# Kernel tuning notes

Measured on AMD Instinct MI355X. Metric: run time of the kernel, lower is better.

Reference implementation:

```python
import jax, jax.numpy as jnp
import numpy as np

N = 8192
IN_DIM = 256
HID = 256
OUT_DIM = 256
P_DIM = 3
SIGMA = 1.0


def setup_inputs() -> dict:
    key = jax.random.key(0)
    ks = jax.random.split(key, 7)
    s_in = 1.0 / np.sqrt(IN_DIM)
    inp = {
        "X": jax.random.normal(ks[0], (N, IN_DIM + P_DIM), dtype=jnp.float32),
        "WQ": jax.random.uniform(ks[1], (IN_DIM, HID), jnp.float32, -s_in, s_in),
        "bQ": jax.random.uniform(ks[2], (HID,), jnp.float32, -s_in, s_in),
        "WK": jax.random.uniform(ks[3], (IN_DIM, HID), jnp.float32, -s_in, s_in),
        "bK": jax.random.uniform(ks[4], (HID,), jnp.float32, -s_in, s_in),
        "WV": jax.random.uniform(ks[5], (IN_DIM, OUT_DIM), jnp.float32, -s_in, s_in),
        "bV": jax.random.uniform(ks[6], (OUT_DIM,), jnp.float32, -s_in, s_in),
    }
    return inp


def _softmax_one(x):
    # exp(x - max) / (1 + sum(exp(x - max))) -- faithful to the torch softmax_one
    m = jnp.max(x, axis=-1, keepdims=True)
    e = jnp.exp(x - m)
    return e / (1.0 + jnp.sum(e, axis=-1, keepdims=True))


def reference(X, WQ, bQ, WK, bK, WV, bV):
    P = X[:, -P_DIM:]            # [N, 3] spatial coords
    Xf = X[:, :-P_DIM]           # [N, IN_DIM] features

    Q = Xf @ WQ + bQ             # [N, HID]
    K = Xf @ WK + bK             # [N, HID]
    V = Xf @ WV + bV             # [N, OUT_DIM]

    scores = (Q @ K.T) / jnp.sqrt(jnp.asarray(HID, Xf.dtype))  # [N, N]

    # squared pairwise distances ||P_i - P_j||^2 (cdist(P,P)**2)
    sq = jnp.sum(P * P, axis=-1)                                # [N]
    d2 = jnp.maximum(sq[:, None] + sq[None, :] - 2.0 * (P @ P.T), 0.0)
    decay = jnp.exp(-d2 / (2.0 * SIGMA ** 2))                   # [N, N]

    A = _softmax_one(scores * decay)                             # [N, N]
    H = A @ V                                                    # [N, OUT_DIM]
    # residual: input_dim == output_dim so res_proj is None
    return H + Xf
```

## Files before the change

kernel.cpp:

```cpp
#include <hip/hip_runtime.h>
#include <hip/hip_bf16.h>
#include <stdint.h>

#define NTOK 8192
#define XSTRIDE 259
#define LOG2E 1.4426950408889634f
#define DECC (-3.4712336270551023f)
#define BN 32

typedef __bf16 bf16x8 __attribute__((ext_vector_type(8)));
typedef float f32x4 __attribute__((ext_vector_type(4)));
typedef float f32x16 __attribute__((ext_vector_type(16)));
typedef unsigned short u16;

union BF8 { u16 u[8]; bf16x8 v; };
union PW  { uint32_t u[4]; bf16x8 v; };

__device__ __forceinline__ u16 f2bf(float f) {
  uint32_t u = __float_as_uint(f);
  u += 0x7FFFu + ((u >> 16) & 1u);
  return (u16)(u >> 16);
}
__device__ __forceinline__ float bf2f(u16 h) {
  return __uint_as_float(((uint32_t)h) << 16);
}
__device__ __forceinline__ float exp2_hw(float x) {
  float r; asm("v_exp_f32 %0, %1" : "=v"(r) : "v"(x)); return r;
}
__device__ __forceinline__ f32x4 mfma16(bf16x8 a, bf16x8 b, f32x4 c) {
  return __builtin_amdgcn_mfma_f32_16x16x32_bf16(a, b, c, 0, 0, 0);
}
__device__ __forceinline__ f32x16 mfma32(bf16x8 a, bf16x8 b, f32x16 c) {
  return __builtin_amdgcn_mfma_f32_32x32x16_bf16(a, b, c, 0, 0, 0);
}
__device__ __forceinline__ void async16(const void* g, void* l) {
  __builtin_amdgcn_global_load_lds(
      (const __attribute__((address_space(1))) uint32_t*)g,
      (__attribute__((address_space(3))) uint32_t*)l, 16, 0, 0);
}
__device__ __forceinline__ void bsplit(float v, u16& h, u16& l) {
  h = f2bf(v);
  l = f2bf(v - bf2f(h));
}

__global__ __launch_bounds__(256) void pos_kernel(
    const float* __restrict__ X, u16* __restrict__ Qp, u16* __restrict__ Kp) {
  const int r = blockIdx.x * 256 + threadIdx.x;
  const float* xp = X + (size_t)r * XSTRIDE + 256;
  const float x = xp[0], y = xp[1], z = xp[2];
  const float w = 0.5f * (x * x + y * y + z * z);
  u16 xh, xl, yh, yl, zh, zl, wh, wl;
  bsplit(x, xh, xl); bsplit(y, yh, yl); bsplit(z, zh, zl); bsplit(w, wh, wl);
  const u16 one = 0x3F80u;
  const u16 SGN = 0x8000u;
  union { u16 u[16]; uint4 v4[2]; } uq, uk;
  uq.u[0] = wh;  uk.u[0] = one;
  uq.u[1] = wl;  uk.u[1] = one;
  uq.u[2] = one; uk.u[2] = wh;
  uq.u[3] = one; uk.u[3] = wl;
  uq.u[4] = (u16)(xh ^ SGN); uk.u[4] = xh;
  uq.u[5] = (u16)(xh ^ SGN); uk.u[5] = xl;
  uq.u[6] = (u16)(xl ^ SGN); uk.u[6] = xh;
  uq.u[7] = (u16)(yh ^ SGN); uk.u[7] = yh;
  uq.u[8] = (u16)(yh ^ SGN); uk.u[8] = yl;
  uq.u[9] = (u16)(yl ^ SGN); uk.u[9] = yh;
  uq.u[10] = (u16)(zh ^ SGN); uk.u[10] = zh;
  uq.u[11] = (u16)(zh ^ SGN); uk.u[11] = zl;
  uq.u[12] = (u16)(zl ^ SGN); uk.u[12] = zh;
  uq.u[13] = 0; uk.u[13] = 0;
  uq.u[14] = 0; uk.u[14] = 0;
  uq.u[15] = 0; uk.u[15] = 0;
  ((uint4*)Qp)[r * 2] = uq.v4[0];
  ((uint4*)Qp)[r * 2 + 1] = uq.v4[1];
  ((uint4*)Kp)[r * 2] = uk.v4[0];
  ((uint4*)Kp)[r * 2 + 1] = uk.v4[1];
}

__global__ __launch_bounds__(256) void xb_kernel(
    const float* __restrict__ X, u16* __restrict__ Xb) {
  const int t = threadIdx.x;
  const int row = blockIdx.x * 8 + (t >> 5);
  const int c0 = (t & 31) * 8;
  const float* xp = X + (size_t)row * XSTRIDE + c0;
  union { u16 u[8]; uint4 v; } o;
#pragma unroll
  for (int j = 0; j < 8; ++j) o.u[j] = f2bf(xp[j]);
  *(uint4*)(Xb + (size_t)row * 256 + c0) = o.v;
}

__global__ __launch_bounds__(256) void wprep_kernel(
    const float* __restrict__ WQ, const float* __restrict__ WK,
    const float* __restrict__ WV, u16* __restrict__ Wt) {
  const int o = blockIdx.x;
  const int which = o >> 8, oo = o & 255;
  const float* W = (which == 0) ? WQ : ((which == 1) ? WK : WV);
  const int k = threadIdx.x;
  Wt[(size_t)o * 256 + k] = f2bf(W[(size_t)k * 256 + oo]);
}

__global__ __launch_bounds__(256) void qkv_kernel(
    const u16* __restrict__ Xb, const u16* __restrict__ Wt,
    const float* __restrict__ bQ, const float* __restrict__ bK,
    const float* __restrict__ bV,
    u16* __restrict__ Qb, u16* __restrict__ Kb, u16* __restrict__ Vt) {
  __shared__ u16 wt[64 * 256];
  const int tid = threadIdx.x;
  const int lane = tid & 63;
  const int wave = tid >> 6;
  const int l15 = lane & 15;
  const int q4 = lane >> 4;
  const int rb = blockIdx.x;
  const int ch = blockIdx.y;
  const int which = ch >> 2;
  const int c0 = (ch & 3) * 64;
  const float* bias = (which == 0) ? bQ : ((which == 1) ? bK : bV);

  bf16x8 xa[2][8];
#pragma unroll
  for (int mt = 0; mt < 2; ++mt) {
    const int row = rb * 128 + wave * 32 + mt * 16 + l15;
#pragma unroll
    for (int kc = 0; kc < 8; ++kc)
      xa[mt][kc] = *(const bf16x8*)(Xb + (size_t)row * 256 + kc * 32 + q4 * 8);
  }
  {
    const u16* Wsrc = Wt + (size_t)(which * 256 + c0) * 256;
    const int rb0 = wave * 16;
#pragma unroll
    for (int i = 0; i < 8; ++i) {
      int r = rb0 + i * 2 + (lane >> 5);
      int c = (lane & 31) ^ (r & 7);
      async16(Wsrc + (size_t)r * 256 + c * 8, wt + (rb0 + i * 2) * 256);
    }
  }
  asm volatile("s_waitcnt vmcnt(0)" ::: "memory");
  __syncthreads();

  f32x4 acc[2][4];
#pragma unroll
  for (int mt = 0; mt < 2; ++mt)
#pragma unroll
    for (int nt = 0; nt < 4; ++nt) acc[mt][nt] = (f32x4){0.f, 0.f, 0.f, 0.f};

#pragma unroll
  for (int kc = 0; kc < 8; ++kc) {
#pragma unroll
    for (int nt = 0; nt < 4; ++nt) {
      bf16x8 wf = *(const bf16x8*)(wt + (nt * 16 + l15) * 256 +
                                   (((kc * 4 + q4) ^ (l15 & 7)) * 8));
#pragma unroll
      for (int mt = 0; mt < 2; ++mt)
        acc[mt][nt] = mfma16(xa[mt][kc], wf, acc[mt][nt]);
    }
  }
  float bc[4];
#pragma unroll
  for (int nt = 0; nt < 4; ++nt) bc[nt] = bias[c0 + nt * 16 + l15];

#pragma unroll
  for (int mt = 0; mt < 2; ++mt)
#pragma unroll
    for (int nt = 0; nt < 4; ++nt)
#pragma unroll
      for (int r = 0; r < 4; ++r) {
        float v = acc[mt][nt][r] + bc[nt];
        int grow = rb * 128 + wave * 32 + mt * 16 + q4 * 4 + r;
        int gc = c0 + nt * 16 + l15;
        if (which == 2)      Vt[(size_t)gc * NTOK + grow] = f2bf(v);
        else if (which == 1) Kb[(size_t)grow * 256 + gc] = f2bf(v);
        else                 Qb[(size_t)((grow >> 5) * 16 + (gc >> 4)) * 512 +
                                ((gc >> 3) & 1) * 256 + (grow & 31) * 8 +
                                (gc & 7)] = f2bf(v);
      }
}

template<int KS>
__global__ __launch_bounds__((KS == 16) ? 512 : 256, 2) void attn_kernel(
    const u16* __restrict__ Qb, const u16* __restrict__ Kb,
    const u16* __restrict__ Vt, const u16* __restrict__ Qp,
    const u16* __restrict__ Kp, u16* __restrict__ Op,
    float* __restrict__ ml) {
  constexpr int WPB = (KS == 16) ? 8 : 4;
  constexpr int KW  = WPB / 2;
  constexpr int SPL = NTOK / KS;
  constexpr int NIT = SPL / BN;
  constexpr int IK  = BN / KW / 2;
  constexpr int FPW = 256 / KW;
  constexpr int IV  = FPW / 16;

  __shared__ u16 kbuf[2][BN * 256];
  __shared__ u16 vbuf[2][256 * BN];
  __shared__ u16 kpbuf[2][BN * 16];

  const int tid = threadIdx.x;
  const int lane = tid & 63;
  const int wave = tid >> 6;
  const int l31 = lane & 31;
  const int h5 = lane >> 5;
  const int sp = blockIdx.x;
  const int rb = blockIdx.y;
  const int q0 = rb * (32 * WPB);
  const int wrow = wave * 32;

#define STAGE(T)                                                              \
  do {                                                                        \
    const int key0_ = sp * SPL + (T) * BN;                                    \
    const int b_ = (T) & 1;                                                   \
    if (wave < KW) {                                                          \
      const int rb0 = wave * (BN / KW);                                       \
      _Pragma("unroll")                                                       \
      for (int i = 0; i < IK; ++i) {                                          \
        int r = rb0 + i * 2 + (lane >> 5);                                    \
        int c = (lane & 31) ^ (r & 7);                                        \
        async16(Kb + (size_t)(key0_ + r) * 256 + c * 8,                       \
                &kbuf[b_][(rb0 + i * 2) * 256]);                              \
      }                                                                       \
      if (wave == 1)                                                          \
        async16(Kp + (size_t)(key0_ + (lane >> 1)) * 16 + (lane & 1) * 8,     \
                &kpbuf[b_][0]);                                               \
    } else {                                                                  \
      const int fb0 = (wave - KW) * FPW;                                      \
      _Pragma("unroll")                                                       \
      for (int i = 0; i < IV; ++i) {                                          \
        int f = fb0 + i * 16 + (lane >> 2);                                   \
        int c = (lane & 3) ^ ((f >> 1) & 3);                                  \
        async16(Vt + (size_t)f * NTOK + key0_ + c * 8,                        \
                &vbuf[b_][(fb0 + i * 16) * 32]);                              \
      }                                                                       \
    }                                                                         \
  } while (0)

  const int rb32 = rb * WPB + wave;
  bf16x8 qa[16];
#pragma unroll
  for (int kc = 0; kc < 16; ++kc)
    qa[kc] = *(const bf16x8*)(Qb + ((size_t)(rb32 * 16 + kc) * 64 + lane) * 8);

  const bf16x8 qp = *(const bf16x8*)(Qp + (size_t)(q0 + wrow + l31) * 16 +
                                     h5 * 8);

  f32x16 O[8];
#pragma unroll
  for (int ft = 0; ft < 8; ++ft)
#pragma unroll
    for (int r = 0; r < 16; ++r) O[ft][r] = 0.f;
  float lrow = 0.f;

  const int kswz = l31 & 7;
  const int vswz = (l31 >> 1) & 3;

  STAGE(0);

#pragma unroll 1
  for (int it = 0; it < NIT; ++it) {
    const int cur = it & 1;
    asm volatile("s_waitcnt vmcnt(0)" ::: "memory");
    __syncthreads();

    const int nx = (it + 1 < NIT) ? (it + 1) : (NIT - 1);
    STAGE(nx);

    f32x16 T;
#pragma unroll
    for (int r = 0; r < 16; ++r) T[r] = 0.f;
    {
      bf16x8 kpf = *(const bf16x8*)(&kpbuf[cur][l31 * 16 + h5 * 8]);
      T = mfma32(kpf, qp, T);
    }

    f32x16 S;
#pragma unroll
    for (int r = 0; r < 16; ++r) S[r] = 0.f;
    __builtin_amdgcn_s_setprio(1);
#pragma unroll
    for (int kc = 0; kc < 16; ++kc) {
      bf16x8 kf = *(const bf16x8*)(&kbuf[cur][l31 * 256 +
                                   (((2 * kc + h5) ^ kswz) * 8)]);
      S = mfma32(kf, qa[kc], S);
    }
    __builtin_amdgcn_s_setprio(0);

#pragma unroll
    for (int r = 0; r < 16; ++r) {
      float dec = exp2_hw(fmaf(T[r], -LOG2E, DECC));
      float p = exp2_hw(S[r] * dec);
      S[r] = p;
      lrow += p;
    }

    uint32_t w0, w1, w2, w3, w4, w5, w6, w7;
    asm("v_cvt_pk_bf16_f32 %0, %1, %2" : "=v"(w0) : "v"(S[0]),  "v"(S[1]));
    asm("v_cvt_pk_bf16_f32 %0, %1, %2" : "=v"(w1) : "v"(S[2]),  "v"(S[3]));
    asm("v_cvt_pk_bf16_f32 %0, %1, %2" : "=v"(w2) : "v"(S[4]),  "v"(S[5]));
    asm("v_cvt_pk_bf16_f32 %0, %1, %2" : "=v"(w3) : "v"(S[6]),  "v"(S[7]));
    asm("v_cvt_pk_bf16_f32 %0, %1, %2" : "=v"(w4) : "v"(S[8]),  "v"(S[9]));
    asm("v_cvt_pk_bf16_f32 %0, %1, %2" : "=v"(w5) : "v"(S[10]), "v"(S[11]));
    asm("v_cvt_pk_bf16_f32 %0, %1, %2" : "=v"(w6) : "v"(S[12]), "v"(S[13]));
    asm("v_cvt_pk_bf16_f32 %0, %1, %2" : "=v"(w7) : "v"(S[14]), "v"(S[15]));
    asm volatile("v_permlane32_swap_b32 %0, %1" : "+v"(w2), "+v"(w0));
    asm volatile("v_permlane32_swap_b32 %0, %1" : "+v"(w3), "+v"(w1));
    asm volatile("v_permlane32_swap_b32 %0, %1" : "+v"(w6), "+v"(w4));
    asm volatile("v_permlane32_swap_b32 %0, %1" : "+v"(w7), "+v"(w5));
    PW pa0, pa1;
    pa0.u[0] = w0; pa0.u[1] = w1; pa0.u[2] = w2; pa0.u[3] = w3;
    pa1.u[0] = w4; pa1.u[1] = w5; pa1.u[2] = w6; pa1.u[3] = w7;

    __builtin_amdgcn_s_setprio(1);
#pragma unroll
    for (int kh = 0; kh < 2; ++kh) {
      const bf16x8 pa = kh ? pa1.v : pa0.v;
#pragma unroll
      for (int ft = 0; ft < 8; ++ft) {
        bf16x8 vf = *(const bf16x8*)(&vbuf[cur][(ft * 32 + l31) * 32 +
                                     (((2 * kh + h5) ^ vswz) * 8)]);
        O[ft] = mfma32(pa, vf, O[ft]);
      }
    }
    __builtin_amdgcn_s_setprio(0);
  }

  float lsum = lrow + __shfl_xor(lrow, 32);
#pragma unroll
  for (int ft = 0; ft < 8; ++ft)
#pragma unroll
    for (int r = 0; r < 16; ++r) {
      int row = q0 + wrow + (r & 3) + 8 * (r >> 2) + 4 * h5;
      Op[((size_t)sp * NTOK + row) * 256 + ft * 32 + l31] = f2bf(O[ft][r]);
    }
  if (lane < 32)
    ml[sp * NTOK + q0 + wrow + lane] = lsum;
#undef STAGE
}

template<int KS>
__global__ __launch_bounds__(256) void combine_kernel(
    const float* __restrict__ X, const u16* __restrict__ Op,
    const float* __restrict__ ml, float* __restrict__ out) {
  const int row = blockIdx.x;
  const int f = threadIdx.x;
  float den = 1.f, num = 0.f;
#pragma unroll
  for (int s = 0; s < KS; ++s) {
    den += ml[s * NTOK + row];
    num += bf2f(Op[((size_t)s * NTOK + row) * 256 + f]);
  }
  out[(size_t)row * 256 + f] = num / den + X[(size_t)row * XSTRIDE + f];
}

extern "C" void kernel_launch(void* const* d_in, const int* in_sizes, int n_in,
                              void* d_out, int out_size, void* d_ws, size_t ws_size,
                              hipStream_t stream) {
  (void)in_sizes; (void)n_in; (void)out_size;
  const float* X  = (const float*)d_in[0];
  const float* WQ = (const float*)d_in[1];
  const float* bQ = (const float*)d_in[2];
  const float* WK = (const float*)d_in[3];
  const float* bK = (const float*)d_in[4];
  const float* WV = (const float*)d_in[5];
  const float* bV = (const float*)d_in[6];
  float* out = (float*)d_out;
  char* ws = (char*)d_ws;

  u16*   Qb = (u16*)(ws);
  u16*   Kb = (u16*)(ws + ((size_t)4 << 20));
  u16*   Vt = (u16*)(ws + ((size_t)8 << 20));
  u16*   Qp = (u16*)(ws + ((size_t)12 << 20));
  u16*   Kp = (u16*)(ws + ((size_t)12 << 20) + 262144);
  u16*   Wt = (u16*)(ws + ((size_t)12 << 20) + 524288);
  u16*   Xb = (u16*)(ws + ((size_t)12 << 20) + 524288 + 393216);
  float* ml = (float*)(ws + ((size_t)16 << 20) + 524288 + 393216);
  u16*   Op = (u16*)(ws + ((size_t)16 << 20) + 524288 + 393216 + 524288);

  const size_t op_off = ((size_t)16 << 20) + 524288 + 393216 + 524288;
  const size_t need16 = op_off + (size_t)16 * NTOK * 256 * 2;
  const bool big = (ws_size >= need16);

  pos_kernel<<<dim3(NTOK / 256), dim3(256), 0, stream>>>(X, Qp, Kp);
  xb_kernel<<<dim3(NTOK / 8), dim3(256), 0, stream>>>(X, Xb);
  wprep_kernel<<<dim3(768), dim3(256), 0, stream>>>(WQ, WK, WV, Wt);
  qkv_kernel<<<dim3(64, 12), dim3(256), 0, stream>>>(Xb, Wt, bQ, bK, bV,
                                                     Qb, Kb, Vt);
  if (big) {
    attn_kernel<16><<<dim3(16, NTOK / 256), dim3(512), 0, stream>>>(
        Qb, Kb, Vt, Qp, Kp, Op, ml);
    combine_kernel<16><<<dim3(NTOK), dim3(256), 0, stream>>>(X, Op, ml, out);
  } else {
    attn_kernel<8><<<dim3(8, NTOK / 128), dim3(256), 0, stream>>>(
        Qb, Kb, Vt, Qp, Kp, Op, ml);
    combine_kernel<8><<<dim3(NTOK), dim3(256), 0, stream>>>(X, Op, ml, out);
  }
}
```

Before: 224.7 us.

## Triple-buffer attention K/V staging with all waves loading and fixed 8-way split

The attention kernel now keeps three LDS buffers and prefetches two tiles ahead. It uses partial vmcnt waits and a plain s_barrier in place of a full drain plus __syncthreads. All eight waves now share K and V loads, where before half the waves loaded K and half loaded V. The key split is fixed at 8 with 256-row blocks, which halves the grid compared with the earlier 16-split path and removes the workspace-size branch. This aims to hide global load latency better, at the cost of more LDS per block (which may limit occupancy) and less grid parallelism.

```diff
diff --git a/kernel.cpp b/kernel.cpp
--- a/kernel.cpp
+++ b/kernel.cpp
@@ -6,7 +6,10 @@
 #define XSTRIDE 259
 #define LOG2E 1.4426950408889634f
 #define DECC (-3.4712336270551023f)
+#define KSPLIT 8
+#define SPLEN (NTOK / KSPLIT)
 #define BN 32
+#define ITERS (SPLEN / BN)
 
 typedef __bf16 bf16x8 __attribute__((ext_vector_type(8)));
 typedef float f32x4 __attribute__((ext_vector_type(4)));
@@ -174,23 +177,14 @@
       }
 }
 
-template<int KS>
-__global__ __launch_bounds__((KS == 16) ? 512 : 256, 2) void attn_kernel(
+__global__ __launch_bounds__(512, 2) void attn_kernel(
     const u16* __restrict__ Qb, const u16* __restrict__ Kb,
     const u16* __restrict__ Vt, const u16* __restrict__ Qp,
     const u16* __restrict__ Kp, u16* __restrict__ Op,
     float* __restrict__ ml) {
-  constexpr int WPB = (KS == 16) ? 8 : 4;
-  constexpr int KW  = WPB / 2;
-  constexpr int SPL = NTOK / KS;
-  constexpr int NIT = SPL / BN;
-  constexpr int IK  = BN / KW / 2;
-  constexpr int FPW = 256 / KW;
-  constexpr int IV  = FPW / 16;
-
-  __shared__ u16 kbuf[2][BN * 256];
-  __shared__ u16 vbuf[2][256 * BN];
-  __shared__ u16 kpbuf[2][BN * 16];
+  __shared__ u16 kbuf[3][BN * 256];
+  __shared__ u16 vbuf[3][256 * BN];
+  __shared__ u16 kpbuf[3][BN * 16];
 
   const int tid = threadIdx.x;
   const int lane = tid & 63;
@@ -199,38 +193,32 @@
   const int h5 = lane >> 5;
   const int sp = blockIdx.x;
   const int rb = blockIdx.y;
-  const int q0 = rb * (32 * WPB);
+  const int q0 = rb * 256;
   const int wrow = wave * 32;
 
-#define STAGE(T)                                                              \
+#define STAGE(T, S_)                                                          \
   do {                                                                        \
-    const int key0_ = sp * SPL + (T) * BN;                                    \
-    const int b_ = (T) & 1;                                                   \
-    if (wave < KW) {                                                          \
-      const int rb0 = wave * (BN / KW);                                       \
-      _Pragma("unroll")                                                       \
-      for (int i = 0; i < IK; ++i) {                                          \
-        int r = rb0 + i * 2 + (lane >> 5);                                    \
-        int c = (lane & 31) ^ (r & 7);                                        \
-        async16(Kb + (size_t)(key0_ + r) * 256 + c * 8,                       \
-                &kbuf[b_][(rb0 + i * 2) * 256]);                              \
-      }                                                                       \
-      if (wave == 1)                                                          \
-        async16(Kp + (size_t)(key0_ + (lane >> 1)) * 16 + (lane & 1) * 8,     \
-                &kpbuf[b_][0]);                                               \
-    } else {                                                                  \
-      const int fb0 = (wave - KW) * FPW;                                      \
-      _Pragma("unroll")                                                       \
-      for (int i = 0; i < IV; ++i) {                                          \
-        int f = fb0 + i * 16 + (lane >> 2);                                   \
-        int c = (lane & 3) ^ ((f >> 1) & 3);                                  \
-        async16(Vt + (size_t)f * NTOK + key0_ + c * 8,                        \
-                &vbuf[b_][(fb0 + i * 16) * 32]);                              \
-      }                                                                       \
+    const int key0_ = sp * SPLEN + (T) * BN;                                  \
+    _Pragma("unroll")                                                         \
+    for (int j = 0; j < 2; ++j) {                                             \
+      int r = wave * 4 + j * 2 + (lane >> 5);                                 \
+      int c = (lane & 31) ^ (r & 7);                                          \
+      async16(Kb + (size_t)(key0_ + r) * 256 + c * 8,                         \
+              &kbuf[S_][(wave * 4 + j * 2) * 256]);                           \
     }                                                                         \
+    _Pragma("unroll")                                                         \
+    for (int j = 0; j < 2; ++j) {                                             \
+      int f = wave * 32 + j * 16 + (lane >> 2);                               \
+      int c = (lane & 3) ^ ((f >> 1) & 3);                                    \
+      async16(Vt + (size_t)f * NTOK + key0_ + c * 8,                          \
+              &vbuf[S_][(wave * 32 + j * 16) * 32]);                          \
+    }                                                                         \
+    if (wave == 0)                                                            \
+      async16(Kp + (size_t)(key0_ + (lane >> 1)) * 16 + (lane & 1) * 8,       \
+              &kpbuf[S_][0]);                                                 \
   } while (0)
 
-  const int rb32 = rb * WPB + wave;
+  const int rb32 = rb * 8 + wave;
   bf16x8 qa[16];
 #pragma unroll
   for (int kc = 0; kc < 16; ++kc)
@@ -249,16 +237,24 @@
   const int kswz = l31 & 7;
   const int vswz = (l31 >> 1) & 3;
 
-  STAGE(0);
-
+  STAGE(0, 0);
+  STAGE(1, 1);
+
+  int cur = 0;
 #pragma unroll 1
-  for (int it = 0; it < NIT; ++it) {
-    const int cur = it & 1;
-    asm volatile("s_waitcnt vmcnt(0)" ::: "memory");
-    __syncthreads();
-
-    const int nx = (it + 1 < NIT) ? (it + 1) : (NIT - 1);
-    STAGE(nx);
+  for (int t = 0; t < ITERS; ++t) {
+    if (t + 1 < ITERS) {
+      if (wave == 0) asm volatile("s_waitcnt vmcnt(5)" ::: "memory");
+      else           asm volatile("s_waitcnt vmcnt(4)" ::: "memory");
+    } else {
+      asm volatile("s_waitcnt vmcnt(0)" ::: "memory");
+    }
+    __builtin_amdgcn_s_barrier();
+
+    if (t + 2 < ITERS) {
+      const int s2 = (cur >= 1) ? (cur - 1) : 2;
+      STAGE(t + 2, s2);
+    }
 
     f32x16 T;
 #pragma unroll
@@ -317,6 +313,8 @@
       }
     }
     __builtin_amdgcn_s_setprio(0);
+
+    cur = (cur == 2) ? 0 : (cur + 1);
   }
 
   float lsum = lrow + __shfl_xor(lrow, 32);
@@ -332,7 +330,6 @@
 #undef STAGE
 }
 
-template<int KS>
 __global__ __launch_bounds__(256) void combine_kernel(
     const float* __restrict__ X, const u16* __restrict__ Op,
     const float* __restrict__ ml, float* __restrict__ out) {
@@ -340,7 +337,7 @@
   const int f = threadIdx.x;
   float den = 1.f, num = 0.f;
 #pragma unroll
-  for (int s = 0; s < KS; ++s) {
+  for (int s = 0; s < KSPLIT; ++s) {
     den += ml[s * NTOK + row];
     num += bf2f(Op[((size_t)s * NTOK + row) * 256 + f]);
   }
@@ -350,7 +347,7 @@
 extern "C" void kernel_launch(void* const* d_in, const int* in_sizes, int n_in,
                               void* d_out, int out_size, void* d_ws, size_t ws_size,
                               hipStream_t stream) {
-  (void)in_sizes; (void)n_in; (void)out_size;
+  (void)in_sizes; (void)n_in; (void)out_size; (void)ws_size;
   const float* X  = (const float*)d_in[0];
   const float* WQ = (const float*)d_in[1];
   const float* bQ = (const float*)d_in[2];
@@ -371,22 +368,12 @@
   float* ml = (float*)(ws + ((size_t)16 << 20) + 524288 + 393216);
   u16*   Op = (u16*)(ws + ((size_t)16 << 20) + 524288 + 393216 + 524288);
 
-  const size_t op_off = ((size_t)16 << 20) + 524288 + 393216 + 524288;
-  const size_t need16 = op_off + (size_t)16 * NTOK * 256 * 2;
-  const bool big = (ws_size >= need16);
-
   pos_kernel<<<dim3(NTOK / 256), dim3(256), 0, stream>>>(X, Qp, Kp);
   xb_kernel<<<dim3(NTOK / 8), dim3(256), 0, stream>>>(X, Xb);
   wprep_kernel<<<dim3(768), dim3(256), 0, stream>>>(WQ, WK, WV, Wt);
   qkv_kernel<<<dim3(64, 12), dim3(256), 0, stream>>>(Xb, Wt, bQ, bK, bV,
                                                      Qb, Kb, Vt);
-  if (big) {
-    attn_kernel<16><<<dim3(16, NTOK / 256), dim3(512), 0, stream>>>(
-        Qb, Kb, Vt, Qp, Kp, Op, ml);
-    combine_kernel<16><<<dim3(NTOK), dim3(256), 0, stream>>>(X, Op, ml, out);
-  } else {
-    attn_kernel<8><<<dim3(8, NTOK / 128), dim3(256), 0, stream>>>(
-        Qb, Kb, Vt, Qp, Kp, Op, ml);
-    combine_kernel<8><<<dim3(NTOK), dim3(256), 0, stream>>>(X, Op, ml, out);
-  }
-}
+  attn_kernel<<<dim3(KSPLIT, NTOK / 256), dim3(512), 0, stream>>>(
+      Qb, Kb, Vt, Qp, Kp, Op, ml);
+  combine_kernel<<<dim3(NTOK), dim3(256), 0, stream>>>(X, Op, ml, out);
+}
```

Result: faster. 208.7 us (-7.1%).
